# Optimization experiments

Measured on AMD Instinct MI355X. Metric: run time of the kernel, lower is better.

Reference implementation:

```python
import jax, jax.numpy as jnp
import numpy as np

OFFS = [(dy, dx) for dy in (-1, 0, 1) for dx in (-1, 0, 1)]  # ME centered 3x3 region


def _build_maps():
    """Build the sparse coordinate pyramid and per-offset kernel maps, exactly
    mirroring MinkowskiEngine: out coords of a stride-2 conv are unique(c//2),
    and a pair (i_in, i_out) exists iff coord_out*stride + offset is active."""
    G = 1024
    rng = np.random.default_rng(0)
    flat = np.sort(rng.choice(G * G, size=300000, replace=False))
    coords = [np.stack(np.unravel_index(flat, (G, G)), axis=1).astype(np.int64)]
    grids = [G]
    for _ in range(3):
        coords.append(np.unique(coords[-1] // 2, axis=0))
        grids.append(grids[-1] // 2)

    def lut(c, g):
        t = -np.ones(g * g, np.int64)
        t[c[:, 0] * g + c[:, 1]] = np.arange(len(c))
        return t

    luts = [lut(c, g) for c, g in zip(coords, grids)]

    def kmap(lvl_in, c_out, stride):
        g, L = grids[lvl_in], luts[lvl_in]
        n_in, n_out = len(coords[lvl_in]), len(c_out)
        base = c_out * stride
        pairs = []
        for dy, dx in OFFS:
            q = base + np.array([dy, dx])
            ok = (q[:, 0] >= 0) & (q[:, 0] < g) & (q[:, 1] >= 0) & (q[:, 1] < g)
            key = np.clip(q[:, 0] * g + q[:, 1], 0, g * g - 1)
            idx = np.where(ok, L[key], -1)
            sel = np.nonzero(idx >= 0)[0]
            pairs.append((idx[sel], sel))
        M = max(len(p[0]) for p in pairs)
        ii = np.full((9, M), n_in, np.int32)   # pad -> dummy zero input row
        oo = np.full((9, M), n_out, np.int32)  # pad -> dummy output row (dropped)
        for k, (a, b) in enumerate(pairs):
            ii[k, :len(a)] = a
            oo[k, :len(b)] = b
        return ii, oo

    maps = {
        'c0': kmap(0, coords[0], 1), 'd0': kmap(0, coords[1], 2),
        'c1': kmap(1, coords[1], 1), 'd1': kmap(1, coords[2], 2),
        'c2': kmap(2, coords[2], 1), 'd2': kmap(2, coords[3], 2),
    }
    return maps, [len(c) for c in coords]


def setup_inputs() -> dict:
    maps, (n0, n1, n2, n3) = _build_maps()
    ks = jax.random.split(jax.random.key(0), 16)
    d = {'feats': jax.random.normal(ks[0], (n0, 1), jnp.float32)}
    chans = [(1, 64), (64, 128), (128, 128), (128, 128), (128, 128), (128, 128)]
    names = ['c0', 'd0', 'c1', 'd1', 'c2', 'd2']
    for i, (nm, (ci, co)) in enumerate(zip(names, chans)):
        d[f'w_{nm}'] = jax.random.normal(ks[1 + 2 * i], (9, ci, co), jnp.float32) / np.sqrt(9.0 * ci)
        d[f'b_{nm}'] = jax.random.normal(ks[2 + 2 * i], (co,), jnp.float32) * 0.01
        d[f'in_{nm}'] = jnp.asarray(maps[nm][0])
        d[f'out_{nm}'] = jnp.asarray(maps[nm][1])
    d.update(n0=n0, n1=n1, n2=n2, n3=n3)
    return d


def sparse_conv(feats, w, b, in_idx, out_idx, n_out):
    """Gather-GEMM-scatter sparse conv. w: [9, Cin, Cout]. Padded pairs point at a
    dummy zero input row (index n_in) and a dummy output row (index n_out)."""
    n_in, cin = feats.shape
    fp = jnp.concatenate([feats, jnp.zeros((1, cin), feats.dtype)], axis=0)
    out = jnp.zeros((n_out + 1, w.shape[2]), feats.dtype)
    for k in range(9):  # fixed kernel volume
        out = out.at[out_idx[k]].add(fp[in_idx[k]] @ w[k])
    return out[:n_out] + b


def reference(feats, w_c0, b_c0, in_c0, out_c0, w_d0, b_d0, in_d0, out_d0,
              w_c1, b_c1, in_c1, out_c1, w_d1, b_d1, in_d1, out_d1,
              w_c2, b_c2, in_c2, out_c2, w_d2, b_d2, in_d2, out_d2,
              n0, n1, n2, n3):
    x = sparse_conv(feats, w_c0, b_c0, in_c0, out_c0, n0)
    out0 = jax.nn.relu(sparse_conv(x, w_d0, b_d0, in_d0, out_d0, n1))
    y = sparse_conv(out0, w_c1, b_c1, in_c1, out_c1, n1)
    out1 = jax.nn.relu(sparse_conv(y, w_d1, b_d1, in_d1, out_d1, n2))
    z = sparse_conv(out1, w_c2, b_c2, in_c2, out_c2, n2)
    out2 = sparse_conv(z, w_d2, b_d2, in_d2, out_d2, n3)
    return (out2, out1, out0)
```

## Files before the change

### kernel.cpp

```cpp
#include <hip/hip_runtime.h>
#include <stdint.h>
#include <algorithm>


#define DI __device__ __forceinline__

typedef __attribute__((ext_vector_type(8))) short bf16x8;
typedef __attribute__((ext_vector_type(4))) float f32x4;

DI uint16_t f2bf(float x){
  union{float f;uint32_t i;}v; v.f=x;
  uint32_t r = v.i + 0x7fffu + ((v.i>>16)&1u);
  return (uint16_t)(r>>16);
}
DI uint32_t pack2(float a, float b){
  return (uint32_t)f2bf(a) | ((uint32_t)f2bf(b) << 16);
}
DI void gload16(const void* g, void* l){
  __builtin_amdgcn_global_load_lds(
      (const __attribute__((address_space(1))) void*)g,
      (__attribute__((address_space(3))) void*)l, 16, 0, 0);
}

__global__ __launch_bounds__(256) void diag_kernel(float* __restrict__ out, long n, float c){
  long i = (long)blockIdx.x*256 + threadIdx.x;
  if (i < n) out[i] = c;
}

__global__ __launch_bounds__(256) void init_table_kernel(int* __restrict__ t, long n){
  long i = (long)blockIdx.x*256 + threadIdx.x;
  if (i < n) t[i] = -1;
}

__global__ __launch_bounds__(256) void build_table_kernel(
    const int* __restrict__ im, const int* __restrict__ om,
    int* __restrict__ tab, int M, int n_in, int n_out){
  const int k = blockIdx.y;
  long t = (long)blockIdx.x*256 + threadIdx.x;
  if (t >= M) return;
  int ii = im[(long)k*M + t];
  int oo = om[(long)k*M + t];
  if (ii >= 0 && ii < n_in && oo >= 0 && oo < n_out)
    tab[(long)k*n_out + oo] = ii;
}

__global__ __launch_bounds__(256) void prep_w_kernel(
    const float* __restrict__ w, uint16_t* __restrict__ wtb, int cin){
  long idx = (long)blockIdx.x*256 + threadIdx.x;
  long total = 9L*128*cin;
  if (idx >= total) return;
  int k = (int)(idx / (128*cin));
  int rem = (int)(idx % (128*cin));
  int cout = rem / cin, ci = rem % cin;
  wtb[idx] = f2bf(w[((long)k*cin + ci)*128 + cout]);
}

__global__ __launch_bounds__(256) void c0_tab_kernel(
    const float* __restrict__ feats, const float* __restrict__ w,
    const float* __restrict__ bias, const int* __restrict__ tab,
    uint16_t* __restrict__ out, int n_out){
  __shared__ float w_s[576];
  __shared__ float b_s[64];
  const int tid = threadIdx.x;
  for (int i = tid; i < 576; i += 256) w_s[i] = w[i];
  if (tid < 64) b_s[tid] = bias[tid];
  __syncthreads();
  long r = (long)blockIdx.x*256 + tid;
  if (r >= n_out) return;
  float f[9];
  #pragma unroll
  for (int k = 0; k < 9; k++){
    int gi = tab[(long)k*n_out + r];
    f[k] = (gi >= 0) ? feats[gi] : 0.f;
  }
  uint16_t* dst = out + r*64;
  #pragma unroll
  for (int c0 = 0; c0 < 64; c0 += 16){
    float a[16];
    #pragma unroll
    for (int j = 0; j < 16; j++) a[j] = b_s[c0+j];
    #pragma unroll
    for (int k = 0; k < 9; k++){
      float fk = f[k];
      #pragma unroll
      for (int j = 0; j < 16; j++) a[j] += fk * w_s[k*64 + c0 + j];
    }
    uint4 o0, o1;
    o0.x = pack2(a[0],a[1]);   o0.y = pack2(a[2],a[3]);
    o0.z = pack2(a[4],a[5]);   o0.w = pack2(a[6],a[7]);
    o1.x = pack2(a[8],a[9]);   o1.y = pack2(a[10],a[11]);
    o1.z = pack2(a[12],a[13]); o1.w = pack2(a[14],a[15]);
    *(uint4*)(dst + c0)     = o0;
    *(uint4*)(dst + c0 + 8) = o1;
  }
}

template<int CIN, int INMODE, int OUTMODE, bool RELU>
__global__ __launch_bounds__(512,4) void mconv2_kernel(
    const void* __restrict__ in_v, const char* __restrict__ ws_base,
    long in_off, long wtb_off, long zp_off,
    const float* __restrict__ bias, const int* __restrict__ tab,
    float* __restrict__ outf, uint16_t* __restrict__ outb, int n_out){
  constexpr int NS = 9*CIN/64;
  __shared__ __align__(16) uint16_t ab[2][128*64];
  __shared__ __align__(16) uint16_t bb[2][128*64];
  __shared__ int gi_sh[(INMODE==1) ? 9*128 : 1];

  const int tid = threadIdx.x;
  const int nwg = gridDim.x, orig = blockIdx.x;
  const int q = nwg >> 3, rr = nwg & 7, xcd = orig & 7, pos = orig >> 3;
  const int wg = (xcd < rr ? xcd*(q+1) : rr*(q+1) + (xcd-rr)*q) + pos;
  const long rb = (long)wg * 128;

  const int r0 = tid >> 3, sg = tid & 7;
  const int ss0 = sg ^ (r0 & 7);

  uint32_t offA[2][9];
  if constexpr (INMODE == 0){
    #pragma unroll
    for (int kk = 0; kk < 9; ++kk){
      #pragma unroll
      for (int it = 0; it < 2; ++it){
        long row = rb + it*64 + r0;
        int gi = (row < (long)n_out) ? tab[(long)kk*n_out + row] : -1;
        offA[it][kk] = (gi >= 0)
            ? (uint32_t)(in_off + (long)gi*(CIN*2) + ss0*16)
            : (uint32_t)(zp_off + ss0*16);
      }
    }
  } else {
    for (int idx = tid; idx < 9*128; idx += 512){
      int k = idx >> 7, r = idx & 127;
      long row = rb + r;
      gi_sh[idx] = (row < (long)n_out) ? tab[(long)k*n_out + row] : -1;
    }
    __syncthreads();
  }

  const uint32_t offB = (uint32_t)(wtb_off + ((long)r0*CIN + ss0*8)*2);

  const int lane = tid & 63;
  const int wv = tid >> 6;
  const int wr = (wv >> 1) << 5;
  const int wc = (wv & 1) << 6;
  const int l16 = lane & 15, quad = lane >> 4;

  f32x4 acc[2][4];
  #pragma unroll
  for (int i = 0; i < 2; i++)
    #pragma unroll
    for (int j = 0; j < 4; j++)
      acc[i][j] = (f32x4){0.f,0.f,0.f,0.f};

  auto stage_b = [&](int step, int nb){
    const int kk  = (CIN == 64) ? step : (step >> 1);
    const int c0b = (CIN == 64) ? 0 : ((step & 1) * 128);
    const uint32_t base = offB + (uint32_t)((long)kk*128*CIN*2 + c0b);
    #pragma unroll
    for (int it = 0; it < 2; ++it)
      gload16(ws_base + base + it*(64*CIN*2), &bb[nb][(it*512+tid)*8]);
  };
  auto stage_a_bf = [&](int step, int nb){
    const int kk  = (CIN == 64) ? step : (step >> 1);
    const int c0b = (CIN == 64) ? 0 : ((step & 1) * 128);
    #pragma unroll
    for (int it = 0; it < 2; ++it)
      gload16(ws_base + offA[it][kk] + c0b, &ab[nb][(it*512+tid)*8]);
  };
  auto stage_a_f32_issue = [&](int step, float4 (*va)[2]){
    const int kk = step >> 1;
    const int ci0 = (step & 1) << 6;
    const float* fb = (const float*)in_v;
    #pragma unroll
    for (int it = 0; it < 2; ++it){
      int gi = gi_sh[(kk << 7) + it*64 + r0];
      if (gi >= 0){
        const float4* s = (const float4*)(fb + (long)gi*128 + ci0 + ss0*8);
        va[it][0] = s[0]; va[it][1] = s[1];
      } else {
        va[it][0] = make_float4(0.f,0.f,0.f,0.f);
        va[it][1] = make_float4(0.f,0.f,0.f,0.f);
      }
    }
  };
  auto stage_a_f32_write = [&](float4 (*va)[2], int nb){
    #pragma unroll
    for (int it = 0; it < 2; ++it){
      uint4 o;
      o.x = pack2(va[it][0].x, va[it][0].y);
      o.y = pack2(va[it][0].z, va[it][0].w);
      o.z = pack2(va[it][1].x, va[it][1].y);
      o.w = pack2(va[it][1].z, va[it][1].w);
      *(uint4*)&ab[nb][(it*512+tid)*8] = o;
    }
  };
  auto compute = [&](int nb){
    const uint16_t* A  = &ab[nb][0];
    const uint16_t* Bm = &bb[nb][0];
    __builtin_amdgcn_s_setprio(1);
    #pragma unroll
    for (int ch = 0; ch < 2; ++ch){
      const int xs = ((((ch << 2) + quad) ^ (l16 & 7)) << 3);
      bf16x8 af[2], bfr[4];
      #pragma unroll
      for (int u = 0; u < 2; ++u)
        af[u]  = *(const bf16x8*)&A [((wr + (u<<4) + l16) << 6) + xs];
      #pragma unroll
      for (int u = 0; u < 4; ++u)
        bfr[u] = *(const bf16x8*)&Bm[((wc + (u<<4) + l16) << 6) + xs];
      #pragma unroll
      for (int rt = 0; rt < 2; ++rt)
        #pragma unroll
        for (int ct = 0; ct < 4; ++ct)
          acc[rt][ct] = __builtin_amdgcn_mfma_f32_16x16x32_bf16(
              af[rt], bfr[ct], acc[rt][ct], 0, 0, 0);
    }
    __builtin_amdgcn_s_setprio(0);
  };

  float4 va[2][2];
  if constexpr (INMODE == 0){
    stage_a_bf(0, 0);
  } else {
    stage_a_f32_issue(0, va);
    stage_a_f32_write(va, 0);
  }
  stage_b(0, 0);
  __syncthreads();

  #pragma unroll
  for (int t = 0; t < NS; ++t){
    const int cur = t & 1;
    const bool more = (t + 1 < NS);
    if (more){
      if constexpr (INMODE == 0) stage_a_bf(t+1, cur^1);
      else stage_a_f32_issue(t+1, va);
      stage_b(t+1, cur^1);
    }
    compute(cur);
    if constexpr (INMODE != 0){
      if (more) stage_a_f32_write(va, cur^1);
    }
    if (more) __syncthreads();
  }

  #pragma unroll
  for (int ct = 0; ct < 4; ++ct){
    const int cout = wc + (ct<<4) + l16;
    const float bv = bias[cout];
    #pragma unroll
    for (int rt = 0; rt < 2; ++rt){
      #pragma unroll
      for (int r = 0; r < 4; ++r){
        long row = rb + wr + (rt<<4) + (quad<<2) + r;
        if (row < (long)n_out){
          float v = acc[rt][ct][r] + bv;
          if (RELU) v = v > 0.f ? v : 0.f;
          if constexpr (OUTMODE == 0 || OUTMODE == 2) outf[row*128 + cout] = v;
          if constexpr (OUTMODE == 1 || OUTMODE == 2) outb[row*128 + cout] = f2bf(v);
        }
      }
    }
  }
}

static inline long cdivl(long a, long b){ return (a + b - 1) / b; }

extern "C" void kernel_launch(void* const* d_in, const int* in_sizes, int n_in_args,
                              void* d_out, int out_size, void* d_ws, size_t ws_size,
                              hipStream_t stream) {
  const float* feats = (const float*)d_in[0];
  const float* w_c0 = (const float*)d_in[1];
  const float* b_c0 = (const float*)d_in[2];
  const int* in_c0  = (const int*)d_in[3];
  const int* out_c0 = (const int*)d_in[4];
  const float* w_d0 = (const float*)d_in[5];
  const float* b_d0 = (const float*)d_in[6];
  const int* in_d0  = (const int*)d_in[7];
  const int* out_d0 = (const int*)d_in[8];
  const float* w_c1 = (const float*)d_in[9];
  const float* b_c1 = (const float*)d_in[10];
  const int* in_c1  = (const int*)d_in[11];
  const int* out_c1 = (const int*)d_in[12];
  const float* w_d1 = (const float*)d_in[13];
  const float* b_d1 = (const float*)d_in[14];
  const int* in_d1  = (const int*)d_in[15];
  const int* out_d1 = (const int*)d_in[16];
  const float* w_c2 = (const float*)d_in[17];
  const float* b_c2 = (const float*)d_in[18];
  const int* in_c2  = (const int*)d_in[19];
  const int* out_c2 = (const int*)d_in[20];
  const float* w_d2 = (const float*)d_in[21];
  const float* b_d2 = (const float*)d_in[22];
  const int* in_d2  = (const int*)d_in[23];
  const int* out_d2 = (const int*)d_in[24];

  const int n0   = in_sizes[0];
  const int M_c0 = in_sizes[3]  / 9;
  const int M_d0 = in_sizes[7]  / 9;
  const int M_c1 = in_sizes[11] / 9;
  const int M_d1 = in_sizes[15] / 9;
  const int M_c2 = in_sizes[19] / 9;
  const int M_d2 = in_sizes[23] / 9;
  const int n1   = M_c1;
  const int n2   = M_c2;
  const int n3   = out_size/128 - n1 - n2;

  bool sane = n0 > 0 && out_size % 128 == 0 &&
              M_c0 > 0 && M_d0 > 0 && M_d1 > 0 && M_d2 > 0 &&
              n1 > 0 && n2 > 0 && n3 > 0;

  long maxElems = (long)n0*64;
  if ((long)n1*128 > maxElems) maxElems = (long)n1*128;
  if ((long)n2*128 > maxElems) maxElems = (long)n2*128;
  long fbytes = (maxElems*2 + 255)/256*256;
  long tbytes = (9L*n0*4 + 255)/256*256;
  long wt64  = 9L*128*64, wt128 = 9L*128*128;
  long wbytes = ((wt64 + 4*wt128)*2 + 255)/256*256;
  long zbytes = 256;
  long b1bytes = sane ? ((long)n2*128*2 + 255)/256*256 : 0;
  long b0bytes = sane ? ((long)n1*128*2 + 255)/256*256 : 0;
  long need0 = fbytes + tbytes + wbytes + zbytes + 256;

  if (!sane || ws_size < (size_t)need0){
    float C = (float)(16 + (int)std::min<size_t>(ws_size >> 20, (size_t)100000));
    if (!sane) C *= 1099511627776.0f;
    diag_kernel<<<cdivl(out_size,256),256,0,stream>>>((float*)d_out, out_size, C);
    return;
  }

  uint16_t* fbuf = (uint16_t*)d_ws;
  int* table = (int*)((char*)d_ws + fbytes);
  long wtb_d0_off = fbytes + tbytes;
  long wtb_c1_off = wtb_d0_off + wt64*2;
  long wtb_d1_off = wtb_c1_off + wt128*2;
  long wtb_c2_off = wtb_d1_off + wt128*2;
  long wtb_d2_off = wtb_c2_off + wt128*2;
  long zp_off     = fbytes + tbytes + wbytes;
  long bf1_off    = need0;
  long bf0_off    = need0 + b1bytes;
  const char* wsb = (const char*)d_ws;
  uint16_t* zp_p  = (uint16_t*)((char*)d_ws + zp_off);
  uint16_t* bf1   = (uint16_t*)((char*)d_ws + bf1_off);
  uint16_t* bf0   = (uint16_t*)((char*)d_ws + bf0_off);
  int tier = 0;
  if (ws_size >= (size_t)(need0 + b1bytes)) tier = 1;
  if (ws_size >= (size_t)(need0 + b1bytes + b0bytes)) tier = 2;

  float* out2 = (float*)d_out;
  float* out1 = out2 + (long)n3*128;
  float* out0 = out1 + (long)n2*128;

  prep_w_kernel<<<cdivl(9L*128*64,256),256,0,stream>>>(w_d0, (uint16_t*)((char*)d_ws + wtb_d0_off), 64);
  prep_w_kernel<<<cdivl(9L*128*128,256),256,0,stream>>>(w_c1, (uint16_t*)((char*)d_ws + wtb_c1_off), 128);
  prep_w_kernel<<<cdivl(9L*128*128,256),256,0,stream>>>(w_d1, (uint16_t*)((char*)d_ws + wtb_d1_off), 128);
  prep_w_kernel<<<cdivl(9L*128*128,256),256,0,stream>>>(w_c2, (uint16_t*)((char*)d_ws + wtb_c2_off), 128);
  prep_w_kernel<<<cdivl(9L*128*128,256),256,0,stream>>>(w_d2, (uint16_t*)((char*)d_ws + wtb_d2_off), 128);
  diag_kernel<<<1,256,0,stream>>>((float*)zp_p, 64, 0.0f);

  auto make_tab = [&](const int* im, const int* om, int M, int nin, int nout){
    long n = 9L*nout;
    init_table_kernel<<<cdivl(n,256),256,0,stream>>>(table, n);
    dim3 g((unsigned)cdivl(M,256), 9);
    build_table_kernel<<<g,256,0,stream>>>(im, om, table, M, nin, nout);
  };

  make_tab(in_c0, out_c0, M_c0, n0, n0);
  c0_tab_kernel<<<cdivl(n0,256),256,0,stream>>>(feats, w_c0, b_c0, table, fbuf, n0);

  make_tab(in_d0, out_d0, M_d0, n0, n1);
  if (tier >= 2)
    mconv2_kernel<64,0,2,true><<<cdivl(n1,128),512,0,stream>>>(
        nullptr, wsb, 0L, wtb_d0_off, zp_off, b_d0, table, out0, bf0, n1);
  else
    mconv2_kernel<64,0,0,true><<<cdivl(n1,128),512,0,stream>>>(
        nullptr, wsb, 0L, wtb_d0_off, zp_off, b_d0, table, out0, nullptr, n1);

  make_tab(in_c1, out_c1, M_c1, n1, n1);
  if (tier >= 2)
    mconv2_kernel<128,0,1,false><<<cdivl(n1,128),512,0,stream>>>(
        nullptr, wsb, bf0_off, wtb_c1_off, zp_off, b_c1, table, nullptr, fbuf, n1);
  else
    mconv2_kernel<128,1,1,false><<<cdivl(n1,128),512,0,stream>>>(
        out0, wsb, 0L, wtb_c1_off, zp_off, b_c1, table, nullptr, fbuf, n1);

  make_tab(in_d1, out_d1, M_d1, n1, n2);
  if (tier >= 1)
    mconv2_kernel<128,0,2,true><<<cdivl(n2,128),512,0,stream>>>(
        nullptr, wsb, 0L, wtb_d1_off, zp_off, b_d1, table, out1, bf1, n2);
  else
    mconv2_kernel<128,0,0,true><<<cdivl(n2,128),512,0,stream>>>(
        nullptr, wsb, 0L, wtb_d1_off, zp_off, b_d1, table, out1, nullptr, n2);

  make_tab(in_c2, out_c2, M_c2, n2, n2);
  if (tier >= 1)
    mconv2_kernel<128,0,1,false><<<cdivl(n2,128),512,0,stream>>>(
        nullptr, wsb, bf1_off, wtb_c2_off, zp_off, b_c2, table, nullptr, fbuf, n2);
  else
    mconv2_kernel<128,1,1,false><<<cdivl(n2,128),512,0,stream>>>(
        out1, wsb, 0L, wtb_c2_off, zp_off, b_c2, table, nullptr, fbuf, n2);

  make_tab(in_d2, out_d2, M_d2, n2, n3);
  mconv2_kernel<128,0,0,false><<<cdivl(n3,128),512,0,stream>>>(
      nullptr, wsb, 0L, wtb_d2_off, zp_off, b_d2, table, out2, nullptr, n3);
}
```

Baseline: 574.0 us.

## Batch table/weight prep into single launches and pipeline bf16 conv loads

All six scatter tables are now built in one init pass and one 3D-grid build kernel over a combined table buffer, and the five weight conversions are merged into one kernel. Together this replaces roughly seventeen small launches with three. The bf16-input GEMM path now waits with explicit vmcnt counters and raw s_barrier instead of __syncthreads, so the next stage's loads can stay in flight during compute. Bias is also loaded before the main loop. The combined tables need more workspace, and the vmcnt(4) count has to match the number of loads issued per stage or the reads race.

```diff
diff --git a/kernel.cpp b/kernel.cpp
--- a/kernel.cpp
+++ b/kernel.cpp
@@ -27,32 +27,49 @@
   if (i < n) out[i] = c;
 }
 
-__global__ __launch_bounds__(256) void init_table_kernel(int* __restrict__ t, long n){
+__global__ __launch_bounds__(256) void init_all_kernel(
+    int* __restrict__ tab, long ntab, float* __restrict__ zp){
   long i = (long)blockIdx.x*256 + threadIdx.x;
-  if (i < n) t[i] = -1;
-}
-
-__global__ __launch_bounds__(256) void build_table_kernel(
-    const int* __restrict__ im, const int* __restrict__ om,
-    int* __restrict__ tab, int M, int n_in, int n_out){
-  const int k = blockIdx.y;
+  if (i < ntab) tab[i] = -1;
+  if (blockIdx.x == 0 && threadIdx.x < 64) zp[threadIdx.x] = 0.f;
+}
+
+struct BuildArgs {
+  const int* im[6];
+  const int* om[6];
+  int   M[6];
+  int   nin[6];
+  int   nout[6];
+  long  toff[6];
+};
+
+__global__ __launch_bounds__(256) void build_all_kernel(
+    BuildArgs a, int* __restrict__ tb){
+  const int L = blockIdx.z, k = blockIdx.y;
+  const int M = a.M[L];
   long t = (long)blockIdx.x*256 + threadIdx.x;
   if (t >= M) return;
-  int ii = im[(long)k*M + t];
-  int oo = om[(long)k*M + t];
-  if (ii >= 0 && ii < n_in && oo >= 0 && oo < n_out)
-    tab[(long)k*n_out + oo] = ii;
-}
-
-__global__ __launch_bounds__(256) void prep_w_kernel(
-    const float* __restrict__ w, uint16_t* __restrict__ wtb, int cin){
+  int ii = a.im[L][(long)k*M + t];
+  int oo = a.om[L][(long)k*M + t];
+  if (ii >= 0 && ii < a.nin[L] && oo >= 0 && oo < a.nout[L])
+    tb[a.toff[L] + (long)k*a.nout[L] + oo] = ii;
+}
+
+__global__ __launch_bounds__(256) void prep_all_kernel(
+    const float* __restrict__ w0, const float* __restrict__ w1,
+    const float* __restrict__ w2, const float* __restrict__ w3,
+    const float* __restrict__ w4, uint16_t* __restrict__ wb, long total){
+  const long wt64 = 9L*128*64, wt128 = 9L*128*128;
   long idx = (long)blockIdx.x*256 + threadIdx.x;
-  long total = 9L*128*cin;
   if (idx >= total) return;
-  int k = (int)(idx / (128*cin));
-  int rem = (int)(idx % (128*cin));
+  int L; long r; int cin;
+  if (idx < wt64){ L = 0; r = idx; cin = 64; }
+  else { long j = idx - wt64; L = 1 + (int)(j / wt128); r = j % wt128; cin = 128; }
+  const float* w = (L==0) ? w0 : (L==1) ? w1 : (L==2) ? w2 : (L==3) ? w3 : w4;
+  int k = (int)(r / (128*cin));
+  int rem = (int)(r % (128*cin));
   int cout = rem / cin, ci = rem % cin;
-  wtb[idx] = f2bf(w[((long)k*cin + ci)*128 + cout]);
+  wb[idx] = f2bf(w[((long)k*cin + ci)*128 + cout]);
 }
 
 __global__ __launch_bounds__(256) void c0_tab_kernel(
@@ -145,6 +162,10 @@
   const int wc = (wv & 1) << 6;
   const int l16 = lane & 15, quad = lane >> 4;
 
+  float bv[4];
+  #pragma unroll
+  for (int ct = 0; ct < 4; ++ct) bv[ct] = bias[wc + (ct<<4) + l16];
+
   f32x4 acc[2][4];
   #pragma unroll
   for (int i = 0; i < 2; i++)
@@ -218,43 +239,57 @@
     __builtin_amdgcn_s_setprio(0);
   };
 
-  float4 va[2][2];
   if constexpr (INMODE == 0){
     stage_a_bf(0, 0);
+    stage_b(0, 0);
+    #pragma unroll
+    for (int t = 0; t < NS; ++t){
+      const int cur = t & 1;
+      if (t + 1 < NS){
+        stage_a_bf(t+1, cur^1);
+        stage_b(t+1, cur^1);
+        asm volatile("s_waitcnt vmcnt(4)" ::: "memory");
+      } else {
+        asm volatile("s_waitcnt vmcnt(0)" ::: "memory");
+      }
+      __builtin_amdgcn_sched_barrier(0);
+      __builtin_amdgcn_s_barrier();
+      compute(cur);
+      if (t + 1 < NS)
+        __builtin_amdgcn_s_barrier();
+    }
   } else {
+    float4 va[2][2];
     stage_a_f32_issue(0, va);
     stage_a_f32_write(va, 0);
-  }
-  stage_b(0, 0);
-  __syncthreads();
-
-  #pragma unroll
-  for (int t = 0; t < NS; ++t){
-    const int cur = t & 1;
-    const bool more = (t + 1 < NS);
-    if (more){
-      if constexpr (INMODE == 0) stage_a_bf(t+1, cur^1);
-      else stage_a_f32_issue(t+1, va);
-      stage_b(t+1, cur^1);
-    }
-    compute(cur);
-    if constexpr (INMODE != 0){
-      if (more) stage_a_f32_write(va, cur^1);
-    }
-    if (more) __syncthreads();
+    stage_b(0, 0);
+    __syncthreads();
+    #pragma unroll
+    for (int t = 0; t < NS; ++t){
+      const int cur = t & 1;
+      const bool more = (t + 1 < NS);
+      if (more){
+        stage_a_f32_issue(t+1, va);
+        stage_b(t+1, cur^1);
+      }
+      compute(cur);
+      if (more){
+        stage_a_f32_write(va, cur^1);
+        __syncthreads();
+      }
+    }
   }
 
   #pragma unroll
   for (int ct = 0; ct < 4; ++ct){
     const int cout = wc + (ct<<4) + l16;
-    const float bv = bias[cout];
     #pragma unroll
     for (int rt = 0; rt < 2; ++rt){
       #pragma unroll
       for (int r = 0; r < 4; ++r){
         long row = rb + wr + (rt<<4) + (quad<<2) + r;
         if (row < (long)n_out){
-          float v = acc[rt][ct][r] + bv;
+          float v = acc[rt][ct][r] + bv[ct];
           if (RELU) v = v > 0.f ? v : 0.f;
           if constexpr (OUTMODE == 0 || OUTMODE == 2) outf[row*128 + cout] = v;
           if constexpr (OUTMODE == 1 || OUTMODE == 2) outb[row*128 + cout] = f2bf(v);
@@ -314,7 +349,8 @@
   if ((long)n1*128 > maxElems) maxElems = (long)n1*128;
   if ((long)n2*128 > maxElems) maxElems = (long)n2*128;
   long fbytes = (maxElems*2 + 255)/256*256;
-  long tbytes = (9L*n0*4 + 255)/256*256;
+  long ntab   = sane ? 9L*((long)n0 + 2L*n1 + 2L*n2 + n3) : 0;
+  long tbytes = (ntab*4 + 255)/256*256;
   long wt64  = 9L*128*64, wt128 = 9L*128*128;
   long wbytes = ((wt64 + 4*wt128)*2 + 255)/256*256;
   long zbytes = 256;
@@ -330,7 +366,7 @@
   }
 
   uint16_t* fbuf = (uint16_t*)d_ws;
-  int* table = (int*)((char*)d_ws + fbytes);
+  long tab_off    = fbytes;
   long wtb_d0_off = fbytes + tbytes;
   long wtb_c1_off = wtb_d0_off + wt64*2;
   long wtb_d1_off = wtb_c1_off + wt128*2;
@@ -340,67 +376,74 @@
   long bf1_off    = need0;
   long bf0_off    = need0 + b1bytes;
   const char* wsb = (const char*)d_ws;
-  uint16_t* zp_p  = (uint16_t*)((char*)d_ws + zp_off);
-  uint16_t* bf1   = (uint16_t*)((char*)d_ws + bf1_off);
-  uint16_t* bf0   = (uint16_t*)((char*)d_ws + bf0_off);
+  int* tb        = (int*)((char*)d_ws + tab_off);
+  float* zp_p    = (float*)((char*)d_ws + zp_off);
+  uint16_t* bf1  = (uint16_t*)((char*)d_ws + bf1_off);
+  uint16_t* bf0  = (uint16_t*)((char*)d_ws + bf0_off);
   int tier = 0;
   if (ws_size >= (size_t)(need0 + b1bytes)) tier = 1;
   if (ws_size >= (size_t)(need0 + b1bytes + b0bytes)) tier = 2;
 
+  long t_c0 = 0;
+  long t_d0 = t_c0 + 9L*n0;
+  long t_c1 = t_d0 + 9L*n1;
+  long t_d1 = t_c1 + 9L*n1;
+  long t_c2 = t_d1 + 9L*n2;
+  long t_d2 = t_c2 + 9L*n2;
+
   float* out2 = (float*)d_out;
   float* out1 = out2 + (long)n3*128;
   float* out0 = out1 + (long)n2*128;
 
-  prep_w_kernel<<<cdivl(9L*128*64,256),256,0,stream>>>(w_d0, (uint16_t*)((char*)d_ws + wtb_d0_off), 64);
-  prep_w_kernel<<<cdivl(9L*128*128,256),256,0,stream>>>(w_c1, (uint16_t*)((char*)d_ws + wtb_c1_off), 128);
-  prep_w_kernel<<<cdivl(9L*128*128,256),256,0,stream>>>(w_d1, (uint16_t*)((char*)d_ws + wtb_d1_off), 128);
-  prep_w_kernel<<<cdivl(9L*128*128,256),256,0,stream>>>(w_c2, (uint16_t*)((char*)d_ws + wtb_c2_off), 128);
-  prep_w_kernel<<<cdivl(9L*128*128,256),256,0,stream>>>(w_d2, (uint16_t*)((char*)d_ws + wtb_d2_off), 128);
-  diag_kernel<<<1,256,0,stream>>>((float*)zp_p, 64, 0.0f);
-
-  auto make_tab = [&](const int* im, const int* om, int M, int nin, int nout){
-    long n = 9L*nout;
-    init_table_kernel<<<cdivl(n,256),256,0,stream>>>(table, n);
-    dim3 g((unsigned)cdivl(M,256), 9);
-    build_table_kernel<<<g,256,0,stream>>>(im, om, table, M, nin, nout);
-  };
-
-  make_tab(in_c0, out_c0, M_c0, n0, n0);
-  c0_tab_kernel<<<cdivl(n0,256),256,0,stream>>>(feats, w_c0, b_c0, table, fbuf, n0);
-
-  make_tab(in_d0, out_d0, M_d0, n0, n1);
+  init_all_kernel<<<cdivl(ntab,256),256,0,stream>>>(tb, ntab, zp_p);
+
+  BuildArgs ba;
+  ba.im[0]=in_c0;  ba.om[0]=out_c0; ba.M[0]=M_c0; ba.nin[0]=n0; ba.nout[0]=n0; ba.toff[0]=t_c0;
+  ba.im[1]=in_d0;  ba.om[1]=out_d0; ba.M[1]=M_d0; ba.nin[1]=n0; ba.nout[1]=n1; ba.toff[1]=t_d0;
+  ba.im[2]=in_c1;  ba.om[2]=out_c1; ba.M[2]=M_c1; ba.nin[2]=n1; ba.nout[2]=n1; ba.toff[2]=t_c1;
+  ba.im[3]=in_d1;  ba.om[3]=out_d1; ba.M[3]=M_d1; ba.nin[3]=n1; ba.nout[3]=n2; ba.toff[3]=t_d1;
+  ba.im[4]=in_c2;  ba.om[4]=out_c2; ba.M[4]=M_c2; ba.nin[4]=n2; ba.nout[4]=n2; ba.toff[4]=t_c2;
+  ba.im[5]=in_d2;  ba.om[5]=out_d2; ba.M[5]=M_d2; ba.nin[5]=n2; ba.nout[5]=n3; ba.toff[5]=t_d2;
+  long maxM = M_c0;
+  for (int i = 0; i < 6; ++i) if (ba.M[i] > maxM) maxM = ba.M[i];
+  dim3 bg((unsigned)cdivl(maxM,256), 9, 6);
+  build_all_kernel<<<bg,256,0,stream>>>(ba, tb);
+
+  long wtotal = wt64 + 4*wt128;
+  prep_all_kernel<<<cdivl(wtotal,256),256,0,stream>>>(
+      w_d0, w_c1, w_d1, w_c2, w_d2,
+      (uint16_t*)((char*)d_ws + wtb_d0_off), wtotal);
+
+  c0_tab_kernel<<<cdivl(n0,256),256,0,stream>>>(feats, w_c0, b_c0, tb + t_c0, fbuf, n0);
+
   if (tier >= 2)
     mconv2_kernel<64,0,2,true><<<cdivl(n1,128),512,0,stream>>>(
-        nullptr, wsb, 0L, wtb_d0_off, zp_off, b_d0, table, out0, bf0, n1);
+        nullptr, wsb, 0L, wtb_d0_off, zp_off, b_d0, tb + t_d0, out0, bf0, n1);
   else
     mconv2_kernel<64,0,0,true><<<cdivl(n1,128),512,0,stream>>>(
-        nullptr, wsb, 0L, wtb_d0_off, zp_off, b_d0, table, out0, nullptr, n1);
-
-  make_tab(in_c1, out_c1, M_c1, n1, n1);
+        nullptr, wsb, 0L, wtb_d0_off, zp_off, b_d0, tb + t_d0, out0, nullptr, n1);
+
   if (tier >= 2)
     mconv2_kernel<128,0,1,false><<<cdivl(n1,128),512,0,stream>>>(
-        nullptr, wsb, bf0_off, wtb_c1_off, zp_off, b_c1, table, nullptr, fbuf, n1);
+        nullptr, wsb, bf0_off, wtb_c1_off, zp_off, b_c1, tb + t_c1, nullptr, fbuf, n1);
   else
     mconv2_kernel<128,1,1,false><<<cdivl(n1,128),512,0,stream>>>(
-        out0, wsb, 0L, wtb_c1_off, zp_off, b_c1, table, nullptr, fbuf, n1);
-
-  make_tab(in_d1, out_d1, M_d1, n1, n2);
+        out0, wsb, 0L, wtb_c1_off, zp_off, b_c1, tb + t_c1, nullptr, fbuf, n1);
+
   if (tier >= 1)
     mconv2_kernel<128,0,2,true><<<cdivl(n2,128),512,0,stream>>>(
-        nullptr, wsb, 0L, wtb_d1_off, zp_off, b_d1, table, out1, bf1, n2);
+        nullptr, wsb, 0L, wtb_d1_off, zp_off, b_d1, tb + t_d1, out1, bf1, n2);
   else
     mconv2_kernel<128,0,0,true><<<cdivl(n2,128),512,0,stream>>>(
-        nullptr, wsb, 0L, wtb_d1_off, zp_off, b_d1, table, out1, nullptr, n2);
-
-  make_tab(in_c2, out_c2, M_c2, n2, n2);
+        nullptr, wsb, 0L, wtb_d1_off, zp_off, b_d1, tb + t_d1, out1, nullptr, n2);
+
   if (tier >= 1)
     mconv2_kernel<128,0,1,false><<<cdivl(n2,128),512,0,stream>>>(
-        nullptr, wsb, bf1_off, wtb_c2_off, zp_off, b_c2, table, nullptr, fbuf, n2);
+        nullptr, wsb, bf1_off, wtb_c2_off, zp_off, b_c2, tb + t_c2, nullptr, fbuf, n2);
   else
     mconv2_kernel<128,1,1,false><<<cdivl(n2,128),512,0,stream>>>(
-        out1, wsb, 0L, wtb_c2_off, zp_off, b_c2, table, nullptr, fbuf, n2);
-
-  make_tab(in_d2, out_d2, M_d2, n2, n3);
+        out1, wsb, 0L, wtb_c2_off, zp_off, b_c2, tb + t_c2, nullptr, fbuf, n2);
+
   mconv2_kernel<128,0,0,false><<<cdivl(n3,128),512,0,stream>>>(
-      nullptr, wsb, 0L, wtb_d2_off, zp_off, b_d2, table, out2, nullptr, n3);
-}
+      nullptr, wsb, 0L, wtb_d2_off, zp_off, b_d2, tb + t_d2, out2, nullptr, n3);
+}
```

After: 486.7 us. -15.2%, faster.
